# Performance work log

Measured on AMD Instinct MI355X. Metric: run time of the kernel, lower is better.

## Reference

```python
import jax, jax.numpy as jnp
import numpy as np

B, MC, U, N, DIN, DOUT, E = 2048, 4, 20000, 100000, 128, 128, 65536
RES_RATE = 0.9


def setup_inputs() -> dict:
    key = jax.random.key(0)
    ks = jax.random.split(key, 12)
    s = 1.0 / np.sqrt(DIN)
    return {
        'nodes': jax.random.randint(ks[0], (B,), 0, N),
        'unique_ids': jax.random.randint(ks[1], (U,), 0, N),
        'row_idx': jnp.repeat(jnp.arange(B), E // B),
        'layer_idx': jax.random.randint(ks[2], (E,), 0, MC),
        'col_idx': jax.random.randint(ks[3], (E,), 0, U),
        'agg_table': jax.random.normal(ks[4], (N, DIN), jnp.float32),
        'ff_table': jax.random.normal(ks[5], (N, DIN), jnp.float32),
        'Wv_agg': jax.random.normal(ks[6], (DIN, DOUT), jnp.float32) * s,
        'Wv_ff': jax.random.normal(ks[7], (DIN, DOUT), jnp.float32) * s,
        'Wk': jax.random.normal(ks[8], (DIN, DOUT), jnp.float32) * s,
        'Wq': jax.random.normal(ks[9], (DIN, DOUT), jnp.float32) * s,
        'mu_w': jax.random.normal(ks[10], (2 * DOUT, 1), jnp.float32) * s,
    }


def reference(nodes, unique_ids, row_idx, layer_idx, col_idx,
              agg_table, ff_table, Wv_agg, Wv_ff, Wk, Wq, mu_w):
    # feature lookups (the 'features' encoder returns (agg_attr, ff_attr))
    embed_agg = agg_table[unique_ids]            # [U, DIN]
    self_agg_raw = agg_table[nodes]              # [B, DIN]
    self_ff_raw = ff_table[nodes]                # [B, DIN]

    # highway K/Q from raw self features
    self_pair = jnp.stack((self_agg_raw, self_ff_raw), axis=1)  # [B, 2, DIN]
    K = self_pair @ Wk                            # [B, 2, DOUT]
    Q = self_pair @ Wq                            # [B, 2, DOUT]

    embed_agg_v = embed_agg @ Wv_agg              # [U, DOUT]
    self_agg = self_agg_raw @ Wv_agg              # [B, DOUT]

    # dense normalized neighbor mask [B, MC, U]
    mask = jnp.zeros((B, MC, U), jnp.float32).at[row_idx, layer_idx, col_idx].set(1.0)
    cnt = mask.sum(-1, keepdims=True)
    mask = mask / jnp.where(cnt == 0, 1.0, cnt)
    neigh = jnp.einsum('bmu,ud->bmd', mask, embed_agg_v)  # [B, MC, DOUT]

    # persona combination
    coef = jnp.concatenate(
        (jnp.broadcast_to(self_agg[:, None, :], (B, MC, DOUT)), neigh), axis=-1)
    norm = jnp.maximum(jnp.linalg.norm(coef, axis=-1, keepdims=True), 1e-12)
    coef = jax.nn.softmax((coef / norm) @ mu_w, axis=1)    # [B, MC, 1]
    neigh_sum = jnp.sum(neigh * coef, axis=1)              # [B, DOUT]
    self_agg = (self_agg + neigh_sum) / 2.0

    # feed-forward branch + highway attention
    self_ff = self_ff_raw @ Wv_ff                          # [B, DOUT]
    V = jnp.stack((self_agg, self_ff), axis=1)             # [B, 2, DOUT]
    scores = jax.nn.softmax(jnp.einsum('bid,bjd->bij', K, Q) / DOUT, axis=-1)
    new = jnp.einsum('bij,bjd->bid', scores, V)            # [B, 2, DOUT]
    self_agg = RES_RATE * self_agg + (1 - RES_RATE) * new[:, 0]
    self_ff = RES_RATE * self_ff + (1 - RES_RATE) * new[:, 1]
    return jax.nn.elu(self_agg), jax.nn.elu(self_ff)
```

## Files before the change

### kernel.cpp

```cpp
#include <hip/hip_runtime.h>
#include <hip/hip_bf16.h>

typedef unsigned short u16;
typedef unsigned int u32;

#define NB 2048
#define NMC 4
#define NU 20000
#define ND 128
#define EPB 32

typedef __attribute__((ext_vector_type(8))) short bf16x8;
typedef __attribute__((ext_vector_type(4))) float f32x4;

__device__ __forceinline__ u32 pack_bf16(float a, float b) {
    __hip_bfloat162 h = __float22bfloat162_rn(make_float2(a, b));
    return *(u32*)&h;
}

__global__ __launch_bounds__(256) void prep_wt(
    const float* __restrict__ Wv_agg, const float* __restrict__ Wk,
    const float* __restrict__ Wq, const float* __restrict__ Wv_ff,
    u16* __restrict__ WT)
{
    __shared__ float Wl[16 * ND];
    const int m = blockIdx.x >> 3;
    const int ks = (blockIdx.x & 7) * 16;
    const int t = threadIdx.x;

    const float* W = (m == 0) ? Wv_agg : (m == 1) ? Wk : (m == 2) ? Wq : Wv_ff;
    const float4* src = (const float4*)(W + ks * ND);
    float4* dst = (float4*)Wl;
    dst[t * 2] = src[t * 2];
    dst[t * 2 + 1] = src[t * 2 + 1];
    __syncthreads();

    const int c = t >> 1, kh = t & 1;
    float v[8];
    #pragma unroll
    for (int j = 0; j < 8; j++) v[j] = Wl[(kh * 8 + j) * ND + c];
    uint4 pk;
    pk.x = pack_bf16(v[0], v[1]);
    pk.y = pack_bf16(v[2], v[3]);
    pk.z = pack_bf16(v[4], v[5]);
    pk.w = pack_bf16(v[6], v[7]);
    *(uint4*)&WT[((size_t)(m * ND + c)) * ND + ks + kh * 8] = pk;
}

#define LDSK 72
#define EMBED_BLOCKS 157

__global__ __launch_bounds__(256) void gemm_all(
    const float* __restrict__ agg, const float* __restrict__ ff,
    const u16* __restrict__ WT,
    const int* __restrict__ uids, const int* __restrict__ nodes,
    float* __restrict__ embed_v,
    float* __restrict__ selfA, float* __restrict__ selfF,
    float* __restrict__ K0, float* __restrict__ K1,
    float* __restrict__ Q0, float* __restrict__ Q1)
{
    __shared__ u16 As[ND * LDSK];
    __shared__ u16 Bs[ND * LDSK];

    const int bx = blockIdx.x;
    const int t  = threadIdx.x;

    const float* table = agg; const int* ids = uids; int wtm = 0;
    float* outp = embed_v;
    int M, r0;
    if (bx < EMBED_BLOCKS) {
        M = NU; r0 = bx * 128;
    } else {
        int z = bx - EMBED_BLOCKS;
        int mode = z >> 4;
        r0 = (z & 15) * 128;
        M = NB; ids = nodes;
        switch (mode) {
            case 0: table = agg; wtm = 0; outp = selfA; break;
            case 1: table = agg; wtm = 1; outp = K0;    break;
            case 2: table = agg; wtm = 2; outp = Q0;    break;
            case 3: table = ff;  wtm = 3; outp = selfF; break;
            case 4: table = ff;  wtm = 1; outp = K1;    break;
            default: table = ff; wtm = 2; outp = Q1;    break;
        }
    }

    const int rs = t >> 1, hs = t & 1;
    int srow = r0 + rs;
    const int id = ids[srow < M ? srow : (M - 1)];
    const float* arow = table + (size_t)id * ND;
    const u16* wrow = WT + ((size_t)(wtm * ND + rs)) * ND;

    const int w = t >> 6, lane = t & 63, q = lane >> 4, li = lane & 15;

    f32x4 acc[2][8];
    #pragma unroll
    for (int i = 0; i < 2; i++)
        #pragma unroll
        for (int j = 0; j < 8; j++) acc[i][j] = (f32x4){0.f, 0.f, 0.f, 0.f};

    for (int pass = 0; pass < 2; pass++) {
        const int k0 = pass * 64;
        {
            const float4* asrc = (const float4*)(arow + k0 + hs * 32);
            #pragma unroll
            for (int i = 0; i < 4; i++) {
                float4 v0 = asrc[2 * i], v1 = asrc[2 * i + 1];
                uint4 pk;
                pk.x = pack_bf16(v0.x, v0.y);
                pk.y = pack_bf16(v0.z, v0.w);
                pk.z = pack_bf16(v1.x, v1.y);
                pk.w = pack_bf16(v1.z, v1.w);
                *(uint4*)&As[rs * LDSK + hs * 32 + i * 8] = pk;
            }
        }
        {
            const uint4* bsrc = (const uint4*)(wrow + k0 + hs * 32);
            #pragma unroll
            for (int i = 0; i < 4; i++)
                *(uint4*)&Bs[rs * LDSK + hs * 32 + i * 8] = bsrc[i];
        }
        __syncthreads();

        #pragma unroll
        for (int c = 0; c < 2; c++) {
            const int kk = c * 32 + q * 8;
            bf16x8 af[2], bfr[8];
            #pragma unroll
            for (int tr = 0; tr < 2; tr++)
                af[tr] = *(const bf16x8*)&As[(w * 32 + tr * 16 + li) * LDSK + kk];
            #pragma unroll
            for (int tc = 0; tc < 8; tc++)
                bfr[tc] = *(const bf16x8*)&Bs[(tc * 16 + li) * LDSK + kk];
            #pragma unroll
            for (int tr = 0; tr < 2; tr++)
                #pragma unroll
                for (int tc = 0; tc < 8; tc++)
                    acc[tr][tc] = __builtin_amdgcn_mfma_f32_16x16x32_bf16(
                        af[tr], bfr[tc], acc[tr][tc], 0, 0, 0);
        }
        __syncthreads();
    }

    #pragma unroll
    for (int tr = 0; tr < 2; tr++) {
        const int rloc = w * 32 + tr * 16 + q * 4;
        #pragma unroll
        for (int r = 0; r < 4; r++) {
            const int row = r0 + rloc + r;
            if (row < M) {
                #pragma unroll
                for (int tc = 0; tc < 8; tc++)
                    outp[(size_t)row * ND + tc * 16 + li] = acc[tr][tc][r];
            }
        }
    }
}

__global__ __launch_bounds__(128) void finalize(
    const int* __restrict__ layer_idx, const int* __restrict__ col_idx,
    const float* __restrict__ embed_v,
    const float* __restrict__ selfA, const float* __restrict__ selfF,
    const float* __restrict__ K0, const float* __restrict__ K1,
    const float* __restrict__ Q0, const float* __restrict__ Q1,
    const float* __restrict__ mu_w, float* __restrict__ out)
{
    const int b = blockIdx.x;
    const int t = threadIdx.x;

    __shared__ int   Ls[EPB], Cs[EPB], cnt[NMC];
    __shared__ float keepf[EPB];
    __shared__ float red[14 * 2];
    __shared__ float bc[8];

    if (t < NMC) cnt[t] = 0;
    if (t < EPB) {
        Ls[t] = layer_idx[b * EPB + t];
        Cs[t] = col_idx[b * EPB + t];
    }
    __syncthreads();
    if (t < EPB) {
        int l = Ls[t], c = Cs[t];
        int kp = 1;
        for (int j = 0; j < t; j++)
            if (Ls[j] == l && Cs[j] == c) { kp = 0; break; }
        keepf[t] = kp ? 1.0f : 0.0f;
        if (kp) atomicAdd(&cnt[l], 1);
    }
    __syncthreads();

    float a0 = 0.f, a1 = 0.f, a2 = 0.f, a3 = 0.f;
    #pragma unroll
    for (int e = 0; e < EPB; e++) {
        float v = embed_v[(size_t)Cs[e] * ND + t];
        float vk = v * keepf[e];
        int l = Ls[e];
        a0 += (l == 0) ? vk : 0.f;
        a1 += (l == 1) ? vk : 0.f;
        a2 += (l == 2) ? vk : 0.f;
        a3 += (l == 3) ? vk : 0.f;
    }
    float inv0 = cnt[0] > 0 ? 1.f / (float)cnt[0] : 0.f;
    float inv1 = cnt[1] > 0 ? 1.f / (float)cnt[1] : 0.f;
    float inv2 = cnt[2] > 0 ? 1.f / (float)cnt[2] : 0.f;
    float inv3 = cnt[3] > 0 ? 1.f / (float)cnt[3] : 0.f;
    float n0 = a0 * inv0, n1 = a1 * inv1, n2 = a2 * inv2, n3 = a3 * inv3;

    const size_t base = (size_t)b * ND + t;
    float sA = selfA[base];
    float sF = selfF[base];
    float k0 = K0[base], k1 = K1[base], q0 = Q0[base], q1 = Q1[base];
    float mu0 = mu_w[t], mu1 = mu_w[ND + t];

    float vals[14] = {
        sA * sA, sA * mu0,
        n0 * n0, n1 * n1, n2 * n2, n3 * n3,
        n0 * mu1, n1 * mu1, n2 * mu1, n3 * mu1,
        k0 * q0, k0 * q1, k1 * q0, k1 * q1
    };
    const int lane = t & 63, wv = t >> 6;
    #pragma unroll
    for (int s = 0; s < 14; s++) {
        float v = vals[s];
        #pragma unroll
        for (int off = 32; off; off >>= 1) v += __shfl_xor(v, off);
        if (lane == 0) red[s * 2 + wv] = v;
    }
    __syncthreads();

    if (t == 0) {
        float sn = red[0] + red[1];
        float ds = red[2] + red[3];
        float sc[NMC], mx = -1e30f;
        #pragma unroll
        for (int m = 0; m < NMC; m++) {
            float nn = red[(2 + m) * 2] + red[(2 + m) * 2 + 1];
            float dn = red[(6 + m) * 2] + red[(6 + m) * 2 + 1];
            float nrm = fmaxf(sqrtf(sn + nn), 1e-12f);
            sc[m] = (ds + dn) / nrm;
            mx = fmaxf(mx, sc[m]);
        }
        float se = 0.f, ee[NMC];
        #pragma unroll
        for (int m = 0; m < NMC; m++) { ee[m] = expf(sc[m] - mx); se += ee[m]; }
        #pragma unroll
        for (int m = 0; m < NMC; m++) bc[m] = ee[m] / se;

        float s00 = (red[20] + red[21]) * (1.f / 128.f);
        float s01 = (red[22] + red[23]) * (1.f / 128.f);
        float s10 = (red[24] + red[25]) * (1.f / 128.f);
        float s11 = (red[26] + red[27]) * (1.f / 128.f);
        float m0 = fmaxf(s00, s01), e00 = expf(s00 - m0), e01 = expf(s01 - m0);
        float d0 = e00 + e01;
        bc[4] = e00 / d0; bc[5] = e01 / d0;
        float m1 = fmaxf(s10, s11), e10 = expf(s10 - m1), e11 = expf(s11 - m1);
        float d1 = e10 + e11;
        bc[6] = e10 / d1; bc[7] = e11 / d1;
    }
    __syncthreads();

    float nsum = n0 * bc[0] + n1 * bc[1] + n2 * bc[2] + n3 * bc[3];
    float sa1 = (sA + nsum) * 0.5f;
    float new0 = bc[4] * sa1 + bc[5] * sF;
    float new1 = bc[6] * sa1 + bc[7] * sF;
    float o0 = 0.9f * sa1 + 0.1f * new0;
    float o1 = 0.9f * sF  + 0.1f * new1;
    o0 = o0 > 0.f ? o0 : (expf(o0) - 1.f);
    o1 = o1 > 0.f ? o1 : (expf(o1) - 1.f);
    out[base] = o0;
    out[(size_t)NB * ND + base] = o1;
}

extern "C" void kernel_launch(void* const* d_in, const int* in_sizes, int n_in,
                              void* d_out, int out_size, void* d_ws, size_t ws_size,
                              hipStream_t stream) {
    const int* nodes  = (const int*)d_in[0];
    const int* uids   = (const int*)d_in[1];
    const int* layer  = (const int*)d_in[3];
    const int* col    = (const int*)d_in[4];
    const float* agg    = (const float*)d_in[5];
    const float* ff     = (const float*)d_in[6];
    const float* Wv_agg = (const float*)d_in[7];
    const float* Wv_ff  = (const float*)d_in[8];
    const float* Wk     = (const float*)d_in[9];
    const float* Wq     = (const float*)d_in[10];
    const float* mu     = (const float*)d_in[11];

    u16*   WT      = (u16*)d_ws;
    float* embed_v = (float*)((char*)d_ws + 4 * ND * ND * sizeof(u16));
    float* selfA   = embed_v + (size_t)NU * ND;
    float* selfF   = selfA + (size_t)NB * ND;
    float* K0      = selfF + (size_t)NB * ND;
    float* K1      = K0 + (size_t)NB * ND;
    float* Q0      = K1 + (size_t)NB * ND;
    float* Q1      = Q0 + (size_t)NB * ND;

    float* out = (float*)d_out;

    prep_wt<<<32, 256, 0, stream>>>(Wv_agg, Wk, Wq, Wv_ff, WT);

    gemm_all<<<EMBED_BLOCKS + 6 * (NB / 128), 256, 0, stream>>>(
        agg, ff, WT, uids, nodes,
        embed_v, selfA, selfF, K0, K1, Q0, Q1);

    finalize<<<NB, 128, 0, stream>>>(
        layer, col, embed_v, selfA, selfF, K0, K1, Q0, Q1, mu, out);
}
```

Before: 152.6 us.

## Store neighbor embeddings as bf16 and run finalize with a single wavefront

The embedding GEMM now writes embed_v as bf16 instead of fp32, which halves its write traffic and the gather traffic in finalize. Finalize is rewritten to use one 64-thread wavefront per batch row, with two columns per thread. Deduplication and per-layer counts use shuffles and ballots instead of shared memory and atomics, and all block reductions become wave reductions with no __syncthreads. Duplicate edges are skipped rather than multiplied by zero. The cost is lower precision in the neighbor embeddings.

```diff
diff --git a/kernel.cpp b/kernel.cpp
--- a/kernel.cpp
+++ b/kernel.cpp
@@ -3,6 +3,7 @@
 
 typedef unsigned short u16;
 typedef unsigned int u32;
+typedef unsigned long long u64;
 
 #define NB 2048
 #define NMC 4
@@ -16,6 +17,15 @@
 __device__ __forceinline__ u32 pack_bf16(float a, float b) {
     __hip_bfloat162 h = __float22bfloat162_rn(make_float2(a, b));
     return *(u32*)&h;
+}
+__device__ __forceinline__ u16 f2bf(float f) {
+    u32 x = __float_as_uint(f);
+    return (u16)((x + 0x7fffu + ((x >> 16) & 1u)) >> 16);
+}
+__device__ __forceinline__ float wsum(float v) {
+    #pragma unroll
+    for (int off = 32; off; off >>= 1) v += __shfl_xor(v, off);
+    return v;
 }
 
 __global__ __launch_bounds__(256) void prep_wt(
@@ -54,7 +64,7 @@
     const float* __restrict__ agg, const float* __restrict__ ff,
     const u16* __restrict__ WT,
     const int* __restrict__ uids, const int* __restrict__ nodes,
-    float* __restrict__ embed_v,
+    u16* __restrict__ embed_bf,
     float* __restrict__ selfA, float* __restrict__ selfF,
     float* __restrict__ K0, float* __restrict__ K1,
     float* __restrict__ Q0, float* __restrict__ Q1)
@@ -66,22 +76,22 @@
     const int t  = threadIdx.x;
 
     const float* table = agg; const int* ids = uids; int wtm = 0;
-    float* outp = embed_v;
+    float* outf = nullptr; u16* outb = nullptr;
     int M, r0;
     if (bx < EMBED_BLOCKS) {
-        M = NU; r0 = bx * 128;
+        M = NU; r0 = bx * 128; outb = embed_bf;
     } else {
         int z = bx - EMBED_BLOCKS;
         int mode = z >> 4;
         r0 = (z & 15) * 128;
         M = NB; ids = nodes;
         switch (mode) {
-            case 0: table = agg; wtm = 0; outp = selfA; break;
-            case 1: table = agg; wtm = 1; outp = K0;    break;
-            case 2: table = agg; wtm = 2; outp = Q0;    break;
-            case 3: table = ff;  wtm = 3; outp = selfF; break;
-            case 4: table = ff;  wtm = 1; outp = K1;    break;
-            default: table = ff; wtm = 2; outp = Q1;    break;
+            case 0: table = agg; wtm = 0; outf = selfA; break;
+            case 1: table = agg; wtm = 1; outf = K0;    break;
+            case 2: table = agg; wtm = 2; outf = Q0;    break;
+            case 3: table = ff;  wtm = 3; outf = selfF; break;
+            case 4: table = ff;  wtm = 1; outf = K1;    break;
+            default: table = ff; wtm = 2; outf = Q1;    break;
         }
     }
 
@@ -149,17 +159,23 @@
         for (int r = 0; r < 4; r++) {
             const int row = r0 + rloc + r;
             if (row < M) {
-                #pragma unroll
-                for (int tc = 0; tc < 8; tc++)
-                    outp[(size_t)row * ND + tc * 16 + li] = acc[tr][tc][r];
+                if (outb) {
+                    #pragma unroll
+                    for (int tc = 0; tc < 8; tc++)
+                        outb[(size_t)row * ND + tc * 16 + li] = f2bf(acc[tr][tc][r]);
+                } else {
+                    #pragma unroll
+                    for (int tc = 0; tc < 8; tc++)
+                        outf[(size_t)row * ND + tc * 16 + li] = acc[tr][tc][r];
+                }
             }
         }
     }
 }
 
-__global__ __launch_bounds__(128) void finalize(
+__global__ __launch_bounds__(64) void finalize(
     const int* __restrict__ layer_idx, const int* __restrict__ col_idx,
-    const float* __restrict__ embed_v,
+    const u16* __restrict__ embed_bf,
     const float* __restrict__ selfA, const float* __restrict__ selfF,
     const float* __restrict__ K0, const float* __restrict__ K1,
     const float* __restrict__ Q0, const float* __restrict__ Q1,
@@ -168,107 +184,106 @@
     const int b = blockIdx.x;
     const int t = threadIdx.x;
 
-    __shared__ int   Ls[EPB], Cs[EPB], cnt[NMC];
-    __shared__ float keepf[EPB];
-    __shared__ float red[14 * 2];
-    __shared__ float bc[8];
-
-    if (t < NMC) cnt[t] = 0;
+    int l = 0, c = 0;
     if (t < EPB) {
-        Ls[t] = layer_idx[b * EPB + t];
-        Cs[t] = col_idx[b * EPB + t];
-    }
-    __syncthreads();
-    if (t < EPB) {
-        int l = Ls[t], c = Cs[t];
-        int kp = 1;
-        for (int j = 0; j < t; j++)
-            if (Ls[j] == l && Cs[j] == c) { kp = 0; break; }
-        keepf[t] = kp ? 1.0f : 0.0f;
-        if (kp) atomicAdd(&cnt[l], 1);
-    }
-    __syncthreads();
-
-    float a0 = 0.f, a1 = 0.f, a2 = 0.f, a3 = 0.f;
+        l = layer_idx[b * EPB + t];
+        c = col_idx[b * EPB + t];
+    }
+    const u32 key = ((u32)l << 15) | (u32)c;
+    int dup = 0;
+    #pragma unroll
+    for (int j = 0; j < EPB; j++) {
+        u32 kj = __shfl(key, j);
+        dup |= (j < t && kj == key);
+    }
+    const int keep = (t < EPB) && !dup;
+    float inv[NMC];
+    #pragma unroll
+    for (int m = 0; m < NMC; m++) {
+        int cm = __popcll(__ballot(keep && (l == m)));
+        inv[m] = cm > 0 ? 1.f / (float)cm : 0.f;
+    }
+    const u32 info = ((u32)c << 3) | ((u32)l << 1) | (u32)keep;
+
+    float a0x = 0.f, a0y = 0.f, a1x = 0.f, a1y = 0.f;
+    float a2x = 0.f, a2y = 0.f, a3x = 0.f, a3y = 0.f;
     #pragma unroll
     for (int e = 0; e < EPB; e++) {
-        float v = embed_v[(size_t)Cs[e] * ND + t];
-        float vk = v * keepf[e];
-        int l = Ls[e];
-        a0 += (l == 0) ? vk : 0.f;
-        a1 += (l == 1) ? vk : 0.f;
-        a2 += (l == 2) ? vk : 0.f;
-        a3 += (l == 3) ? vk : 0.f;
-    }
-    float inv0 = cnt[0] > 0 ? 1.f / (float)cnt[0] : 0.f;
-    float inv1 = cnt[1] > 0 ? 1.f / (float)cnt[1] : 0.f;
-    float inv2 = cnt[2] > 0 ? 1.f / (float)cnt[2] : 0.f;
-    float inv3 = cnt[3] > 0 ? 1.f / (float)cnt[3] : 0.f;
-    float n0 = a0 * inv0, n1 = a1 * inv1, n2 = a2 * inv2, n3 = a3 * inv3;
-
-    const size_t base = (size_t)b * ND + t;
-    float sA = selfA[base];
-    float sF = selfF[base];
-    float k0 = K0[base], k1 = K1[base], q0 = Q0[base], q1 = Q1[base];
-    float mu0 = mu_w[t], mu1 = mu_w[ND + t];
-
-    float vals[14] = {
-        sA * sA, sA * mu0,
-        n0 * n0, n1 * n1, n2 * n2, n3 * n3,
-        n0 * mu1, n1 * mu1, n2 * mu1, n3 * mu1,
-        k0 * q0, k0 * q1, k1 * q0, k1 * q1
-    };
-    const int lane = t & 63, wv = t >> 6;
-    #pragma unroll
-    for (int s = 0; s < 14; s++) {
-        float v = vals[s];
-        #pragma unroll
-        for (int off = 32; off; off >>= 1) v += __shfl_xor(v, off);
-        if (lane == 0) red[s * 2 + wv] = v;
-    }
-    __syncthreads();
-
-    if (t == 0) {
-        float sn = red[0] + red[1];
-        float ds = red[2] + red[3];
-        float sc[NMC], mx = -1e30f;
-        #pragma unroll
-        for (int m = 0; m < NMC; m++) {
-            float nn = red[(2 + m) * 2] + red[(2 + m) * 2 + 1];
-            float dn = red[(6 + m) * 2] + red[(6 + m) * 2 + 1];
-            float nrm = fmaxf(sqrtf(sn + nn), 1e-12f);
-            sc[m] = (ds + dn) / nrm;
-            mx = fmaxf(mx, sc[m]);
-        }
-        float se = 0.f, ee[NMC];
-        #pragma unroll
-        for (int m = 0; m < NMC; m++) { ee[m] = expf(sc[m] - mx); se += ee[m]; }
-        #pragma unroll
-        for (int m = 0; m < NMC; m++) bc[m] = ee[m] / se;
-
-        float s00 = (red[20] + red[21]) * (1.f / 128.f);
-        float s01 = (red[22] + red[23]) * (1.f / 128.f);
-        float s10 = (red[24] + red[25]) * (1.f / 128.f);
-        float s11 = (red[26] + red[27]) * (1.f / 128.f);
-        float m0 = fmaxf(s00, s01), e00 = expf(s00 - m0), e01 = expf(s01 - m0);
-        float d0 = e00 + e01;
-        bc[4] = e00 / d0; bc[5] = e01 / d0;
-        float m1 = fmaxf(s10, s11), e10 = expf(s10 - m1), e11 = expf(s11 - m1);
-        float d1 = e10 + e11;
-        bc[6] = e10 / d1; bc[7] = e11 / d1;
-    }
-    __syncthreads();
-
-    float nsum = n0 * bc[0] + n1 * bc[1] + n2 * bc[2] + n3 * bc[3];
-    float sa1 = (sA + nsum) * 0.5f;
-    float new0 = bc[4] * sa1 + bc[5] * sF;
-    float new1 = bc[6] * sa1 + bc[7] * sF;
-    float o0 = 0.9f * sa1 + 0.1f * new0;
-    float o1 = 0.9f * sF  + 0.1f * new1;
-    o0 = o0 > 0.f ? o0 : (expf(o0) - 1.f);
-    o1 = o1 > 0.f ? o1 : (expf(o1) - 1.f);
-    out[base] = o0;
-    out[(size_t)NB * ND + base] = o1;
+        u32 inf = __shfl(info, e);
+        if (inf & 1u) {
+            int ce = inf >> 3, le = (inf >> 1) & 3;
+            u32 v = *(const u32*)&embed_bf[(size_t)ce * ND + 2 * t];
+            float lo = __uint_as_float(v << 16);
+            float hi = __uint_as_float(v & 0xffff0000u);
+            switch (le) {
+                case 0: a0x += lo; a0y += hi; break;
+                case 1: a1x += lo; a1y += hi; break;
+                case 2: a2x += lo; a2y += hi; break;
+                default: a3x += lo; a3y += hi; break;
+            }
+        }
+    }
+    const float n0x = a0x * inv[0], n0y = a0y * inv[0];
+    const float n1x = a1x * inv[1], n1y = a1y * inv[1];
+    const float n2x = a2x * inv[2], n2y = a2y * inv[2];
+    const float n3x = a3x * inv[3], n3y = a3y * inv[3];
+
+    const size_t base2 = (size_t)b * ND + 2 * t;
+    float2 sA = *(const float2*)&selfA[base2];
+    float2 sF = *(const float2*)&selfF[base2];
+    float2 k0 = *(const float2*)&K0[base2];
+    float2 k1 = *(const float2*)&K1[base2];
+    float2 q0 = *(const float2*)&Q0[base2];
+    float2 q1 = *(const float2*)&Q1[base2];
+    float2 mu0 = *(const float2*)&mu_w[2 * t];
+    float2 mu1 = *(const float2*)&mu_w[ND + 2 * t];
+
+    const float sn = wsum(sA.x * sA.x + sA.y * sA.y);
+    const float ds = wsum(sA.x * mu0.x + sA.y * mu0.y);
+    float nn[NMC], dn[NMC];
+    nn[0] = wsum(n0x * n0x + n0y * n0y); dn[0] = wsum(n0x * mu1.x + n0y * mu1.y);
+    nn[1] = wsum(n1x * n1x + n1y * n1y); dn[1] = wsum(n1x * mu1.x + n1y * mu1.y);
+    nn[2] = wsum(n2x * n2x + n2y * n2y); dn[2] = wsum(n2x * mu1.x + n2y * mu1.y);
+    nn[3] = wsum(n3x * n3x + n3y * n3y); dn[3] = wsum(n3x * mu1.x + n3y * mu1.y);
+    const float s00 = wsum(k0.x * q0.x + k0.y * q0.y) * (1.f / 128.f);
+    const float s01 = wsum(k0.x * q1.x + k0.y * q1.y) * (1.f / 128.f);
+    const float s10 = wsum(k1.x * q0.x + k1.y * q0.y) * (1.f / 128.f);
+    const float s11 = wsum(k1.x * q1.x + k1.y * q1.y) * (1.f / 128.f);
+
+    float sc[NMC], mx = -1e30f;
+    #pragma unroll
+    for (int m = 0; m < NMC; m++) {
+        float nrm = fmaxf(sqrtf(sn + nn[m]), 1e-12f);
+        sc[m] = (ds + dn[m]) / nrm;
+        mx = fmaxf(mx, sc[m]);
+    }
+    float se = 0.f, ee[NMC];
+    #pragma unroll
+    for (int m = 0; m < NMC; m++) { ee[m] = expf(sc[m] - mx); se += ee[m]; }
+    const float ise = 1.f / se;
+    const float bc0 = ee[0] * ise, bc1 = ee[1] * ise;
+    const float bc2 = ee[2] * ise, bc3 = ee[3] * ise;
+
+    const float m0 = fmaxf(s00, s01), e00 = expf(s00 - m0), e01 = expf(s01 - m0);
+    const float id0 = 1.f / (e00 + e01);
+    const float c00 = e00 * id0, c01 = e01 * id0;
+    const float m1 = fmaxf(s10, s11), e10 = expf(s10 - m1), e11 = expf(s11 - m1);
+    const float id1 = 1.f / (e10 + e11);
+    const float c10 = e10 * id1, c11 = e11 * id1;
+
+    const float nsx = n0x * bc0 + n1x * bc1 + n2x * bc2 + n3x * bc3;
+    const float nsy = n0y * bc0 + n1y * bc1 + n2y * bc2 + n3y * bc3;
+    const float sa1x = (sA.x + nsx) * 0.5f, sa1y = (sA.y + nsy) * 0.5f;
+    float o0x = 0.9f * sa1x + 0.1f * (c00 * sa1x + c01 * sF.x);
+    float o0y = 0.9f * sa1y + 0.1f * (c00 * sa1y + c01 * sF.y);
+    float o1x = 0.9f * sF.x + 0.1f * (c10 * sa1x + c11 * sF.x);
+    float o1y = 0.9f * sF.y + 0.1f * (c10 * sa1y + c11 * sF.y);
+    o0x = o0x > 0.f ? o0x : (expf(o0x) - 1.f);
+    o0y = o0y > 0.f ? o0y : (expf(o0y) - 1.f);
+    o1x = o1x > 0.f ? o1x : (expf(o1x) - 1.f);
+    o1y = o1y > 0.f ? o1y : (expf(o1y) - 1.f);
+    *(float2*)&out[base2] = make_float2(o0x, o0y);
+    *(float2*)&out[(size_t)NB * ND + base2] = make_float2(o1x, o1y);
 }
 
 extern "C" void kernel_launch(void* const* d_in, const int* in_sizes, int n_in,
@@ -286,14 +301,15 @@
     const float* Wq     = (const float*)d_in[10];
     const float* mu     = (const float*)d_in[11];
 
-    u16*   WT      = (u16*)d_ws;
-    float* embed_v = (float*)((char*)d_ws + 4 * ND * ND * sizeof(u16));
-    float* selfA   = embed_v + (size_t)NU * ND;
-    float* selfF   = selfA + (size_t)NB * ND;
-    float* K0      = selfF + (size_t)NB * ND;
-    float* K1      = K0 + (size_t)NB * ND;
-    float* Q0      = K1 + (size_t)NB * ND;
-    float* Q1      = Q0 + (size_t)NB * ND;
+    u16*   WT       = (u16*)d_ws;
+    u16*   embed_bf = WT + (size_t)4 * ND * ND;
+    float* fbase    = (float*)(embed_bf + (size_t)NU * ND);
+    float* selfA = fbase;
+    float* selfF = selfA + (size_t)NB * ND;
+    float* K0    = selfF + (size_t)NB * ND;
+    float* K1    = K0 + (size_t)NB * ND;
+    float* Q0    = K1 + (size_t)NB * ND;
+    float* Q1    = Q0 + (size_t)NB * ND;
 
     float* out = (float*)d_out;
 
@@ -301,8 +317,8 @@
 
     gemm_all<<<EMBED_BLOCKS + 6 * (NB / 128), 256, 0, stream>>>(
         agg, ff, WT, uids, nodes,
-        embed_v, selfA, selfF, K0, K1, Q0, Q1);
-
-    finalize<<<NB, 128, 0, stream>>>(
-        layer, col, embed_v, selfA, selfF, K0, K1, Q0, Q1, mu, out);
-}
+        embed_bf, selfA, selfF, K0, K1, Q0, Q1);
+
+    finalize<<<NB, 64, 0, stream>>>(
+        layer, col, embed_bf, selfA, selfF, K0, K1, Q0, Q1, mu, out);
+}
```

New measurement: 153.2 us. About the same (+0.4%).
